# Performance work log

Hardware: AMD Instinct MI355X
Metric: run time of the kernel (lower is better)

Reference implementation:

```python
import math
import jax, jax.numpy as jnp
import numpy as np

D, NH, NL, NP = 256, 8, 4, 4
C = D // NH
VALUE_SHAPES = np.array([[128, 128], [64, 64], [32, 32], [16, 16]], dtype=np.int32)


def _offset_bias():
    # Faithful to MSDeformAttn._reset_parameters grid init for sampling_offsets.bias
    th = np.arange(NH, dtype=np.float32) * (2.0 * np.pi / NH)
    g = np.stack([np.cos(th), np.sin(th)], -1)                      # [NH,2]
    g = g / np.abs(g).max(-1, keepdims=True)
    g = np.tile(g[:, None, None, :], (1, NL, NP, 1))                # [NH,NL,NP,2]
    g = g * np.arange(1, NP + 1, dtype=np.float32)[None, None, :, None]
    return jnp.asarray(g.reshape(-1), jnp.float32)


def setup_inputs() -> dict:
    key = jax.random.key(0)
    ks = jax.random.split(key, 10)
    bs, Q = 8, 2048
    LV = int((VALUE_SHAPES[:, 0] * VALUE_SHAPES[:, 1]).sum())
    s = 0.02
    return {
        "query": jax.random.normal(ks[0], (bs, Q, D), jnp.float32),
        "refer_bbox": jax.random.uniform(ks[1], (bs, Q, NL, 2), jnp.float32),
        "value": jax.random.normal(ks[2], (bs, LV, D), jnp.float32),
        "value_shapes": VALUE_SHAPES,  # static numpy (shapes must be compile-time constants)
        "W_value": jax.random.normal(ks[3], (D, D), jnp.float32) * s,
        "b_value": jnp.zeros((D,), jnp.float32),
        "W_off": jax.random.normal(ks[4], (D, NH * NL * NP * 2), jnp.float32) * 0.01,
        "b_off": _offset_bias(),
        "W_attn": jax.random.normal(ks[5], (D, NH * NL * NP), jnp.float32) * s,
        "b_attn": jnp.zeros((NH * NL * NP,), jnp.float32),
        "W_out": jax.random.normal(ks[6], (D, D), jnp.float32) * s,
        "b_out": jnp.zeros((D,), jnp.float32),
    }


def _ms_deform_attn(value, shapes, loc, attn):
    # value: [bs,LV,NH,C], loc: [bs,Q,NH,NL,NP,2] in [0,1], attn: [bs,Q,NH,NL,NP]
    bs, LV = value.shape[:2]
    Q = loc.shape[1]
    BH = bs * NH
    v = value.transpose(0, 2, 1, 3).reshape(BH, LV, C)              # [BH,LV,C]
    loc = loc.transpose(0, 2, 1, 3, 4, 5).reshape(BH, Q, NL, NP, 2)
    attn = attn.transpose(0, 2, 1, 3, 4).reshape(BH, Q, NL, NP)
    acc = jnp.zeros((BH, Q, C), value.dtype)
    start = 0
    for lvl in range(NL):
        H, W = int(shapes[lvl, 0]), int(shapes[lvl, 1])
        img = v[:, start:start + H * W]                             # [BH,HW,C]
        start += H * W
        # grid_sample(align_corners=False): pixel coord = loc * size - 0.5
        x = loc[:, :, lvl, :, 0] * W - 0.5                          # [BH,Q,NP]
        y = loc[:, :, lvl, :, 1] * H - 0.5
        x0 = jnp.floor(x); y0 = jnp.floor(y)
        fx = x - x0; fy = y - y0
        x0i = x0.astype(jnp.int32); y0i = y0.astype(jnp.int32)
        samp = jnp.zeros((BH, Q, NP, C), value.dtype)
        for dx, dy in ((0, 0), (1, 0), (0, 1), (1, 1)):
            xi = x0i + dx; yi = y0i + dy
            valid = (xi >= 0) & (xi < W) & (yi >= 0) & (yi < H)     # zero padding
            w = (fx if dx else 1.0 - fx) * (fy if dy else 1.0 - fy)
            w = jnp.where(valid, w, 0.0)
            idx = jnp.clip(yi, 0, H - 1) * W + jnp.clip(xi, 0, W - 1)
            g = jnp.take_along_axis(img, idx.reshape(BH, Q * NP)[..., None], axis=1)
            samp = samp + w[..., None] * g.reshape(BH, Q, NP, C)
        acc = acc + (samp * attn[:, :, lvl, :, None]).sum(2)
    return acc.reshape(bs, NH, Q, C).transpose(0, 2, 1, 3).reshape(bs, Q, D)


def reference(query, refer_bbox, value, value_shapes, W_value, b_value,
              W_off, b_off, W_attn, b_attn, W_out, b_out):
    shapes = np.asarray(value_shapes)  # static
    bs, Q = query.shape[:2]
    LV = value.shape[1]
    v = (value @ W_value + b_value).reshape(bs, LV, NH, C)
    off = (query @ W_off + b_off).reshape(bs, Q, NH, NL, NP, 2)
    attn = jax.nn.softmax((query @ W_attn + b_attn).reshape(bs, Q, NH, NL * NP), -1)
    attn = attn.reshape(bs, Q, NH, NL, NP)
    norm = jnp.asarray(shapes[:, ::-1], query.dtype)                # (W,H) per level
    loc = refer_bbox[:, :, None, :, None, :] + off / norm[None, None, None, :, None, :]
    out = _ms_deform_attn(v, shapes, loc, attn)
    return out @ W_out + b_out
```

## Files before the change

### kernel.cpp

```cpp
#include <hip/hip_runtime.h>
#include <hip/hip_bf16.h>

#define D_MODEL 256
#define NHEAD   8
#define NLVL    4
#define NPTS    4
#define CH      32
#define QTOT    2048
#define BS      8
#define LVTOT   21760
#define KDIM    256

typedef __attribute__((ext_vector_type(8))) short bf16x8;
typedef __attribute__((ext_vector_type(4))) float f32x4;

__device__ inline float bf_lo(unsigned u) { unsigned t = u << 16; float f; __builtin_memcpy(&f, &t, 4); return f; }
__device__ inline float bf_hi(unsigned u) { unsigned t = u & 0xffff0000u; float f; __builtin_memcpy(&f, &t, 4); return f; }
__device__ inline float bfu2f(unsigned short s) { unsigned t = (unsigned)s << 16; float f; __builtin_memcpy(&f, &t, 4); return f; }
__device__ inline unsigned short f2bfu(float f) { __hip_bfloat16 h = __float2bfloat16(f); unsigned short u; __builtin_memcpy(&u, &h, 2); return u; }

__global__ __launch_bounds__(256)
void convert_W(const float* __restrict__ W, __hip_bfloat16* __restrict__ Wt, int sh) {
    int t = blockIdx.x * 256 + threadIdx.x;
    int k = t >> sh, n = t & ((1 << sh) - 1);
    Wt[n * 256 + k] = __float2bfloat16(W[(k << sh) + n]);
}

__global__ __launch_bounds__(256)
void convert_q(const float* __restrict__ q, __hip_bfloat16* __restrict__ qb) {
    int t = blockIdx.x * 256 + threadIdx.x;
    float4 f = ((const float4*)q)[t];
    __hip_bfloat16 h4[4] = {__float2bfloat16(f.x), __float2bfloat16(f.y),
                            __float2bfloat16(f.z), __float2bfloat16(f.w)};
    ((uint2*)qb)[t] = *(const uint2*)h4;
}

#define BK  64
#define LDP 72

__global__ __launch_bounds__(256, 2)
void gemm_value_mfma(const float* __restrict__ A,
                     const __hip_bfloat16* __restrict__ Wt,
                     const float* __restrict__ bias,
                     __hip_bfloat16* __restrict__ v) {
    __shared__ __align__(16) __hip_bfloat16 As[128 * LDP];
    __shared__ __align__(16) __hip_bfloat16 Bs[256 * LDP];

    const int tid  = threadIdx.x;
    const int lane = tid & 63;
    const int wave = tid >> 6;
    const int wr   = wave >> 1;
    const int wc   = wave & 1;
    const int rowBase = blockIdx.x * 128;

    const int m0   = lane & 15;
    const int quad = lane >> 4;

    const int sr = tid >> 1;
    const int sk = (tid & 1) * 32;

    f32x4 acc[4][8] = {};

    for (int kc = 0; kc < KDIM; kc += BK) {
        const float* ap = A + (size_t)(rowBase + sr) * KDIM + kc + sk;
#pragma unroll
        for (int j = 0; j < 4; ++j) {
            float4 f0 = *(const float4*)(ap + j * 8);
            float4 f1 = *(const float4*)(ap + j * 8 + 4);
            __align__(16) __hip_bfloat16 t8[8];
            t8[0] = __float2bfloat16(f0.x); t8[1] = __float2bfloat16(f0.y);
            t8[2] = __float2bfloat16(f0.z); t8[3] = __float2bfloat16(f0.w);
            t8[4] = __float2bfloat16(f1.x); t8[5] = __float2bfloat16(f1.y);
            t8[6] = __float2bfloat16(f1.z); t8[7] = __float2bfloat16(f1.w);
            *(uint4*)&As[sr * LDP + sk + j * 8] = *(const uint4*)t8;
        }
        const uint4* bp = (const uint4*)(Wt + (size_t)tid * KDIM + kc);
#pragma unroll
        for (int j = 0; j < 8; ++j)
            *(uint4*)&Bs[tid * LDP + j * 8] = bp[j];
        __syncthreads();

#pragma unroll
        for (int ks = 0; ks < 2; ++ks) {
            bf16x8 af[4], bfv[8];
#pragma unroll
            for (int i = 0; i < 4; ++i)
                af[i] = *(const bf16x8*)&As[(wr * 64 + i * 16 + m0) * LDP + ks * 32 + quad * 8];
#pragma unroll
            for (int j = 0; j < 8; ++j)
                bfv[j] = *(const bf16x8*)&Bs[(wc * 128 + j * 16 + m0) * LDP + ks * 32 + quad * 8];
#pragma unroll
            for (int i = 0; i < 4; ++i)
#pragma unroll
                for (int j = 0; j < 8; ++j)
                    acc[i][j] = __builtin_amdgcn_mfma_f32_16x16x32_bf16(af[i], bfv[j], acc[i][j], 0, 0, 0);
        }
        __syncthreads();
    }

    const int b = rowBase / LVTOT;
    const int pixBase = rowBase - b * LVTOT + wr * 64;
#pragma unroll
    for (int j = 0; j < 8; ++j) {
        const int gcol = wc * 128 + j * 16 + m0;
        const int h = gcol >> 5, c = gcol & 31;
        const float bv = bias[gcol];
        __hip_bfloat16* vp = v + ((size_t)(b * NHEAD + h) * LVTOT) * CH + c;
#pragma unroll
        for (int i = 0; i < 4; ++i) {
            const int pix0 = pixBase + i * 16 + quad * 4;
#pragma unroll
            for (int r = 0; r < 4; ++r)
                vp[(size_t)(pix0 + r) * CH] = __float2bfloat16(acc[i][j][r] + bv);
        }
    }
}

struct StorePlain {
    float* o;
    int ncol;
    __device__ void operator()(int row, int col, float val) const {
        o[(size_t)row * ncol + col] = val;
    }
};

template <typename Store>
__global__ __launch_bounds__(256, 2)
void gemm_bf16_mfma(const __hip_bfloat16* __restrict__ A,
                    const __hip_bfloat16* __restrict__ Wt,
                    const float* __restrict__ bias, Store store) {
    __shared__ __align__(16) __hip_bfloat16 As[128 * LDP];
    __shared__ __align__(16) __hip_bfloat16 Bs[128 * LDP];

    const int tid  = threadIdx.x;
    const int lane = tid & 63;
    const int wave = tid >> 6;
    const int rowBase = blockIdx.x * 128;
    const int cb = blockIdx.y * 128;

    const int m0   = lane & 15;
    const int quad = lane >> 4;

    const int sr = tid >> 1;
    const int sk = (tid & 1) * 32;

    f32x4 acc[2][8] = {};

    for (int kc = 0; kc < KDIM; kc += BK) {
        const uint4* ap = (const uint4*)(A + (size_t)(rowBase + sr) * KDIM + kc + sk);
#pragma unroll
        for (int j = 0; j < 4; ++j)
            *(uint4*)&As[sr * LDP + sk + j * 8] = ap[j];
        const uint4* bp = (const uint4*)(Wt + (size_t)(cb + sr) * KDIM + kc + sk);
#pragma unroll
        for (int j = 0; j < 4; ++j)
            *(uint4*)&Bs[sr * LDP + sk + j * 8] = bp[j];
        __syncthreads();

#pragma unroll
        for (int ks = 0; ks < 2; ++ks) {
            bf16x8 af[2], bfv[8];
#pragma unroll
            for (int i = 0; i < 2; ++i)
                af[i] = *(const bf16x8*)&As[(wave * 32 + i * 16 + m0) * LDP + ks * 32 + quad * 8];
#pragma unroll
            for (int j = 0; j < 8; ++j)
                bfv[j] = *(const bf16x8*)&Bs[(j * 16 + m0) * LDP + ks * 32 + quad * 8];
#pragma unroll
            for (int i = 0; i < 2; ++i)
#pragma unroll
                for (int j = 0; j < 8; ++j)
                    acc[i][j] = __builtin_amdgcn_mfma_f32_16x16x32_bf16(af[i], bfv[j], acc[i][j], 0, 0, 0);
        }
        __syncthreads();
    }

#pragma unroll
    for (int j = 0; j < 8; ++j) {
        const int col = cb + j * 16 + m0;
        const float bv = bias[col];
#pragma unroll
        for (int i = 0; i < 2; ++i) {
            const int row0 = rowBase + wave * 32 + i * 16 + quad * 4;
#pragma unroll
            for (int r = 0; r < 4; ++r)
                store(row0 + r, col, acc[i][j][r] + bv);
        }
    }
}

__global__ __launch_bounds__(256)
void sample_kernel(const float* __restrict__ off_ws,
                   const float* __restrict__ logits_ws,
                   const float* __restrict__ bbox,
                   const __hip_bfloat16* __restrict__ v,
                   __hip_bfloat16* __restrict__ acc_bf) {
    __shared__ __align__(16) float off_s[8 * 256];
    __shared__ __align__(16) float attn_s[8 * 128];
    __shared__ float bbox_s[64];
    __shared__ __align__(16) int idx_s[1024 * 4];
    __shared__ __align__(8) unsigned short w_s[1024 * 4];

    const int tid = threadIdx.x;
    const int b = blockIdx.x & 7;
    const int gq0 = b * QTOT + (blockIdx.x >> 3) * 8;

    const float4* osrc = (const float4*)(off_ws + (size_t)gq0 * 256);
    ((float4*)off_s)[tid] = osrc[tid];
    ((float4*)off_s)[tid + 256] = osrc[tid + 256];
    const float4* lsrc = (const float4*)(logits_ws + (size_t)gq0 * 128);
    ((float4*)attn_s)[tid] = lsrc[tid];
    if (tid < 64) bbox_s[tid] = bbox[(size_t)gq0 * 8 + tid];
    __syncthreads();

    if (tid < 64) {
        int qq = tid >> 3, h = tid & 7;
        float* p = attn_s + qq * 128 + h * 16;
        float m = p[0];
#pragma unroll
        for (int i = 1; i < 16; ++i) m = fmaxf(m, p[i]);
        float e[16], s = 0.f;
#pragma unroll
        for (int i = 0; i < 16; ++i) { e[i] = __expf(p[i] - m); s += e[i]; }
        float inv = 1.f / s;
#pragma unroll
        for (int i = 0; i < 16; ++i) p[i] = e[i] * inv;
    }
    __syncthreads();

#pragma unroll
    for (int r = 0; r < 4; ++r) {
        const int tap = tid + r * 256;
        const int qq = tap >> 7, h = (tap >> 4) & 7, l = (tap >> 2) & 3, p = tap & 3;
        const int Wd = 128 >> l;
        const int st = (l == 0) ? 0 : (l == 1) ? 16384 : (l == 2) ? 20480 : 21504;

        const float bx = bbox_s[qq * 8 + l * 2 + 0];
        const float by = bbox_s[qq * 8 + l * 2 + 1];
        const float ox = off_s[qq * 256 + h * 32 + l * 8 + p * 2 + 0];
        const float oy = off_s[qq * 256 + h * 32 + l * 8 + p * 2 + 1];
        const float att = attn_s[qq * 128 + h * 16 + l * 4 + p];

        const float x = bx * (float)Wd + ox - 0.5f;
        const float y = by * (float)Wd + oy - 0.5f;
        const float x0f = floorf(x), y0f = floorf(y);
        const float fx = x - x0f, fy = y - y0f;
        const int x0 = (int)x0f, y0 = (int)y0f;
        const int x1 = x0 + 1, y1 = y0 + 1;
        const bool vx0 = (unsigned)x0 < (unsigned)Wd;
        const bool vx1 = (unsigned)x1 < (unsigned)Wd;
        const bool vy0 = (unsigned)y0 < (unsigned)Wd;
        const bool vy1 = (unsigned)y1 < (unsigned)Wd;
        const int cx0 = min(max(x0, 0), Wd - 1), cx1 = min(max(x1, 0), Wd - 1);
        const int cy0 = min(max(y0, 0), Wd - 1), cy1 = min(max(y1, 0), Wd - 1);

        int4 idx;
        idx.x = (st + cy0 * Wd + cx0) << 6;
        idx.y = (st + cy0 * Wd + cx1) << 6;
        idx.z = (st + cy1 * Wd + cx0) << 6;
        idx.w = (st + cy1 * Wd + cx1) << 6;
        float w0 = (vx0 && vy0) ? (1.f - fx) * (1.f - fy) * att : 0.f;
        float w1 = (vx1 && vy0) ? fx * (1.f - fy) * att : 0.f;
        float w2 = (vx0 && vy1) ? (1.f - fx) * fy * att : 0.f;
        float w3 = (vx1 && vy1) ? fx * fy * att : 0.f;

        *(int4*)&idx_s[tap * 4] = idx;
        unsigned short w4[4] = {f2bfu(w0), f2bfu(w1), f2bfu(w2), f2bfu(w3)};
        *(uint2*)&w_s[tap * 4] = *(const uint2*)w4;
    }
    __syncthreads();

    const int lane = tid & 63;
    const int wave = tid >> 6;
    const int g = lane >> 4;
    const int c2 = lane & 15;

    const char* vbase = (const char*)v + (size_t)b * NHEAD * LVTOT * (CH * 2) + c2 * 4;

    for (int i = 0; i < 16; ++i) {
        const int pair = wave * 16 + i;
        const int qq = pair >> 3, hh = pair & 7;
        const char* slab = vbase + (size_t)hh * LVTOT * (CH * 2);
        const int tbase = qq * 128 + hh * 16;

        float ax0 = 0.f, ay0 = 0.f, ax1 = 0.f, ay1 = 0.f, ax2 = 0.f, ay2 = 0.f, ax3 = 0.f, ay3 = 0.f;
#pragma unroll
        for (int ts = 0; ts < 4; ++ts) {
            const int tap = tbase + ts * 4 + g;
            const int4 idx = *(const int4*)&idx_s[tap * 4];
            const ushort4 ww = *(const ushort4*)&w_s[tap * 4];
            unsigned u0 = *(const unsigned*)(slab + idx.x);
            unsigned u1 = *(const unsigned*)(slab + idx.y);
            unsigned u2 = *(const unsigned*)(slab + idx.z);
            unsigned u3 = *(const unsigned*)(slab + idx.w);
            float w0 = bfu2f(ww.x), w1 = bfu2f(ww.y), w2 = bfu2f(ww.z), w3 = bfu2f(ww.w);
            ax0 += w0 * bf_lo(u0); ay0 += w0 * bf_hi(u0);
            ax1 += w1 * bf_lo(u1); ay1 += w1 * bf_hi(u1);
            ax2 += w2 * bf_lo(u2); ay2 += w2 * bf_hi(u2);
            ax3 += w3 * bf_lo(u3); ay3 += w3 * bf_hi(u3);
        }
        float sx = (ax0 + ax1) + (ax2 + ax3);
        float sy = (ay0 + ay1) + (ay2 + ay3);
        sx += __shfl_xor(sx, 16); sy += __shfl_xor(sy, 16);
        sx += __shfl_xor(sx, 32); sy += __shfl_xor(sy, 32);
        if (g == 0) {
            __hip_bfloat16 h2[2] = {__float2bfloat16(sx), __float2bfloat16(sy)};
            unsigned packed; __builtin_memcpy(&packed, h2, 4);
            *(unsigned*)((char*)acc_bf + ((size_t)(gq0 + qq) * 256 + hh * 32 + c2 * 2) * 2) = packed;
        }
    }
}

extern "C" void kernel_launch(void* const* d_in, const int* in_sizes, int n_in,
                              void* d_out, int out_size, void* d_ws, size_t ws_size,
                              hipStream_t stream) {
    const float* query   = (const float*)d_in[0];
    const float* bbox    = (const float*)d_in[1];
    const float* value   = (const float*)d_in[2];
    const float* W_value = (const float*)d_in[4];
    const float* b_value = (const float*)d_in[5];
    const float* W_off   = (const float*)d_in[6];
    const float* b_off   = (const float*)d_in[7];
    const float* W_attn  = (const float*)d_in[8];
    const float* b_attn  = (const float*)d_in[9];
    const float* W_out   = (const float*)d_in[10];
    const float* b_out   = (const float*)d_in[11];
    float* out = (float*)d_out;

    char* ws = (char*)d_ws;
    __hip_bfloat16* v_ws  = (__hip_bfloat16*)ws;
    float* off_ws         = (float*)(ws + 89128960);
    float* logits_ws      = (float*)(ws + 89128960 + 16777216);
    __hip_bfloat16* acc_bf = (__hip_bfloat16*)(ws + 89128960 + 16777216 + 8388608);
    __hip_bfloat16* q_bf   = (__hip_bfloat16*)(ws + 89128960 + 16777216 + 8388608 + 8388608);

    __hip_bfloat16* Wt_v    = acc_bf;
    __hip_bfloat16* Wt_off  = acc_bf + 65536;
    __hip_bfloat16* Wt_attn = acc_bf + 131072;
    __hip_bfloat16* Wt_out  = q_bf;

    const int NQ = BS * QTOT;
    const int NVROWS = BS * LVTOT;

    convert_q<<<NQ * KDIM / 1024, 256, 0, stream>>>(query, q_bf);
    convert_W<<<256, 256, 0, stream>>>(W_value, Wt_v, 8);
    convert_W<<<256, 256, 0, stream>>>(W_off, Wt_off, 8);
    convert_W<<<128, 256, 0, stream>>>(W_attn, Wt_attn, 7);

    gemm_value_mfma<<<NVROWS / 128, 256, 0, stream>>>(value, Wt_v, b_value, v_ws);

    gemm_bf16_mfma<<<dim3(NQ / 128, 2), 256, 0, stream>>>(
        q_bf, Wt_off, b_off, StorePlain{off_ws, 256});

    gemm_bf16_mfma<<<dim3(NQ / 128, 1), 256, 0, stream>>>(
        q_bf, Wt_attn, b_attn, StorePlain{logits_ws, 128});

    convert_W<<<256, 256, 0, stream>>>(W_out, Wt_out, 8);

    sample_kernel<<<NQ / 8, 256, 0, stream>>>(off_ws, logits_ws, bbox, v_ws, acc_bf);

    gemm_bf16_mfma<<<dim3(NQ / 128, 2), 256, 0, stream>>>(
        acc_bf, Wt_out, b_out, StorePlain{out, 256});
}
```

Measured before the change: 408.3 us.

## Store projected value in pixel-major layout via LDS-staged coalesced writes

The value projection now writes its output in natural [b, pixel, 256] order instead of head-major [b, head, pixel, 32]. It stages the bf16 tile in shared memory, reusing the A/B buffers, so the writeback becomes coalesced 16-byte stores of contiguous 512-byte rows. The sampling kernel's index stride and head offset change to match. This cuts scattered 2-byte global stores in the GEMM epilogue, but sampling lanes for a given head now read from 512-byte-strided rows, which could change gather locality.

```diff
diff --git a/kernel.cpp b/kernel.cpp
--- a/kernel.cpp
+++ b/kernel.cpp
@@ -37,14 +37,17 @@
 
 #define BK  64
 #define LDP 72
+#define LDC 264
 
 __global__ __launch_bounds__(256, 2)
 void gemm_value_mfma(const float* __restrict__ A,
                      const __hip_bfloat16* __restrict__ Wt,
                      const float* __restrict__ bias,
                      __hip_bfloat16* __restrict__ v) {
-    __shared__ __align__(16) __hip_bfloat16 As[128 * LDP];
-    __shared__ __align__(16) __hip_bfloat16 Bs[256 * LDP];
+    __shared__ __align__(16) char smem[128 * LDC * 2];
+    __hip_bfloat16* As = (__hip_bfloat16*)smem;
+    __hip_bfloat16* Bs = (__hip_bfloat16*)(smem + 128 * LDP * 2);
+    __hip_bfloat16* Cs = (__hip_bfloat16*)smem;
 
     const int tid  = threadIdx.x;
     const int lane = tid & 63;
@@ -99,19 +102,31 @@
     }
 
     const int b = rowBase / LVTOT;
-    const int pixBase = rowBase - b * LVTOT + wr * 64;
+    const int pixBase = rowBase - b * LVTOT;
 #pragma unroll
     for (int j = 0; j < 8; ++j) {
         const int gcol = wc * 128 + j * 16 + m0;
-        const int h = gcol >> 5, c = gcol & 31;
         const float bv = bias[gcol];
-        __hip_bfloat16* vp = v + ((size_t)(b * NHEAD + h) * LVTOT) * CH + c;
 #pragma unroll
         for (int i = 0; i < 4; ++i) {
-            const int pix0 = pixBase + i * 16 + quad * 4;
+            const int lrow = wr * 64 + i * 16 + quad * 4;
 #pragma unroll
             for (int r = 0; r < 4; ++r)
-                vp[(size_t)(pix0 + r) * CH] = __float2bfloat16(acc[i][j][r] + bv);
+                Cs[(lrow + r) * LDC + gcol] = __float2bfloat16(acc[i][j][r] + bv);
+        }
+    }
+    __syncthreads();
+
+    {
+        char* dst = (char*)v + (size_t)(b * LVTOT + pixBase) * 512;
+        const char* src = (const char*)Cs;
+#pragma unroll
+        for (int it = 0; it < 16; ++it) {
+            const int o = it * 4096 + tid * 16;
+            const int row = o >> 9;
+            const int cb  = o & 511;
+            uint4 val = *(const uint4*)(src + row * (LDC * 2) + cb);
+            *(uint4*)(dst + o) = val;
         }
     }
 }
@@ -255,10 +270,10 @@
         const int cy0 = min(max(y0, 0), Wd - 1), cy1 = min(max(y1, 0), Wd - 1);
 
         int4 idx;
-        idx.x = (st + cy0 * Wd + cx0) << 6;
-        idx.y = (st + cy0 * Wd + cx1) << 6;
-        idx.z = (st + cy1 * Wd + cx0) << 6;
-        idx.w = (st + cy1 * Wd + cx1) << 6;
+        idx.x = (st + cy0 * Wd + cx0) << 9;
+        idx.y = (st + cy0 * Wd + cx1) << 9;
+        idx.z = (st + cy1 * Wd + cx0) << 9;
+        idx.w = (st + cy1 * Wd + cx1) << 9;
         float w0 = (vx0 && vy0) ? (1.f - fx) * (1.f - fy) * att : 0.f;
         float w1 = (vx1 && vy0) ? fx * (1.f - fy) * att : 0.f;
         float w2 = (vx0 && vy1) ? (1.f - fx) * fy * att : 0.f;
@@ -275,12 +290,12 @@
     const int g = lane >> 4;
     const int c2 = lane & 15;
 
-    const char* vbase = (const char*)v + (size_t)b * NHEAD * LVTOT * (CH * 2) + c2 * 4;
+    const char* vbase = (const char*)v + (size_t)b * LVTOT * 512 + c2 * 4;
 
     for (int i = 0; i < 16; ++i) {
         const int pair = wave * 16 + i;
         const int qq = pair >> 3, hh = pair & 7;
-        const char* slab = vbase + (size_t)hh * LVTOT * (CH * 2);
+        const char* slab = vbase + hh * 64;
         const int tbase = qq * 128 + hh * 16;
 
         float ax0 = 0.f, ay0 = 0.f, ax1 = 0.f, ay1 = 0.f, ax2 = 0.f, ay2 = 0.f, ax3 = 0.f, ay3 = 0.f;
```

Measured after the change: 408.5 us. No clear change (+0.1%).
